# Performance work log

Measured on AMD Instinct MI355X. Metric: run time of the kernel, lower is better.

## Reference

```python
import jax, jax.numpy as jnp
import numpy as np

INF = 1e9
EPS = 1e-10
LN_EPS = 1e-5
H, CH = 8, 16  # no_heads, c_hidden


def setup_inputs() -> dict:
    key = jax.random.key(0)
    ks = jax.random.split(key, 8)
    B, S, R, C = 1, 2048, 512, 64  # batch, n_seq, n_res, c_in
    sc = 0.02
    m = jax.random.normal(ks[0], (B, S, R, C), jnp.float32)
    mask = jnp.ones((B, S, R), jnp.float32)
    ln_w = jnp.ones((C,), jnp.float32)
    ln_b = jnp.zeros((C,), jnp.float32)
    Wq = jax.random.normal(ks[1], (C, H * CH), jnp.float32) * sc
    Wk = jax.random.normal(ks[2], (C, CH), jnp.float32) * sc
    Wv = jax.random.normal(ks[3], (C, CH), jnp.float32) * sc
    Wg = jax.random.normal(ks[4], (C, H * CH), jnp.float32) * sc
    bg = jnp.ones((H * CH,), jnp.float32)  # gating init: bias = 1
    Wo = jax.random.normal(ks[5], (H * CH, C), jnp.float32) * sc
    bo = jnp.zeros((C,), jnp.float32)
    return {"m": m, "mask": mask, "ln_w": ln_w, "ln_b": ln_b, "Wq": Wq,
            "Wk": Wk, "Wv": Wv, "Wg": Wg, "bg": bg, "Wo": Wo, "bo": bo}


def reference(m, mask, ln_w, ln_b, Wq, Wk, Wv, Wg, bg, Wo, bo):
    # m: [B, S, R, C], mask: [B, S, R]
    m = jnp.swapaxes(m, -2, -3)        # [B, R, S, C] -- attend over seq per column
    mask = jnp.swapaxes(mask, -1, -2)  # [B, R, S]
    # LayerNorm over c_in
    mu = jnp.mean(m, axis=-1, keepdims=True)
    var = jnp.var(m, axis=-1, keepdims=True)
    mn = (m - mu) / jnp.sqrt(var + LN_EPS) * ln_w + ln_b  # [B, R, S, C]
    # masked mean-pooled query over seq dim
    q = jnp.sum(mn * mask[..., None], axis=-2) / (jnp.sum(mask, axis=-1)[..., None] + EPS)  # [B, R, C]
    q = (q @ Wq) * (CH ** -0.5)
    q = q.reshape(*q.shape[:-1], H, CH)  # [B, R, H, CH]
    k = mn @ Wk  # [B, R, S, CH]  (single shared K/V head)
    v = mn @ Wv  # [B, R, S, CH]
    a = jnp.einsum('brhc,brsc->brhs', q, k)
    a = a + (INF * (mask - 1.0))[..., None, :]  # additive mask bias
    a = jax.nn.softmax(a, axis=-1)               # [B, R, H, S]
    o = jnp.einsum('brhs,brsc->brhc', a, v)      # [B, R, H, CH]
    g = jax.nn.sigmoid(mn @ Wg + bg)             # [B, R, S, H*CH]
    g = g.reshape(*g.shape[:-1], H, CH)          # [B, R, S, H, CH]
    o = o[..., None, :, :] * g                   # broadcast pooled attn over seq
    o = o.reshape(*o.shape[:-2], -1)             # [B, R, S, H*CH]
    out = o @ Wo + bo                            # [B, R, S, C]
    return jnp.swapaxes(out, -2, -3)             # [B, S, R, C]
```

## Files before the change

### kernel.cpp

```cpp
#include <hip/hip_runtime.h>
#include <stdint.h>

#define S_ 2048
#define R_ 512
#define C_ 64
#define HC_ 128

typedef unsigned short u16;
typedef __attribute__((ext_vector_type(8))) short bf8_t;
typedef __attribute__((ext_vector_type(4))) float f4_t;

__device__ __forceinline__ u16 f2b(float f) {
    union { float f; unsigned int i; } x; x.f = f;
    unsigned int r = x.i + 0x7fffu + ((x.i >> 16) & 1u);
    return (u16)(r >> 16);
}
__device__ __forceinline__ float b2f(u16 u) {
    union { unsigned int i; float f; } x; x.i = ((unsigned int)u) << 16; return x.f;
}
__device__ __forceinline__ unsigned int pack2(float a, float b) {
    return (unsigned int)f2b(a) | ((unsigned int)f2b(b) << 16);
}
__device__ __forceinline__ void u4_to_f8(uint4 p, float* f) {
    union { unsigned int i; float f; } x;
    x.i = p.x << 16;         f[0] = x.f;
    x.i = p.x & 0xffff0000u; f[1] = x.f;
    x.i = p.y << 16;         f[2] = x.f;
    x.i = p.y & 0xffff0000u; f[3] = x.f;
    x.i = p.z << 16;         f[4] = x.f;
    x.i = p.z & 0xffff0000u; f[5] = x.f;
    x.i = p.w << 16;         f[6] = x.f;
    x.i = p.w & 0xffff0000u; f[7] = x.f;
}

__global__ __launch_bounds__(256) void k1a(
    const float* __restrict__ m, const float* __restrict__ mask,
    const float* __restrict__ lnw_g, const float* __restrict__ lnb_g,
    const float* __restrict__ Wk, const float* __restrict__ Wv,
    u16* __restrict__ kbuf, u16* __restrict__ vbuf,
    float* __restrict__ qsum, float* __restrict__ msum)
{
    __shared__ __attribute__((aligned(16))) u16 mns[32 * 72];
    __shared__ __attribute__((aligned(16))) u16 kvT[32 * 72];
    __shared__ __attribute__((aligned(16))) u16 kva[32 * 40];
    __shared__ float qred[4][64];
    __shared__ float msred[4];

    const int tid = threadIdx.x;
    const int bi  = blockIdx.x;
    const int r   = bi >> 6;
    const int s0  = (bi & 63) << 5;

    for (int idx = tid; idx < 2048; idx += 256) {
        int j = idx & 31, c = idx >> 5;
        float w = (j < 16) ? Wk[c * 16 + j] : Wv[c * 16 + (j - 16)];
        kvT[j * 72 + c] = f2b(w);
    }

    const int g = tid >> 4, l = tid & 15;
    const float4 lw4 = *(const float4*)&lnw_g[4 * l];
    const float4 lb4 = *(const float4*)&lnb_g[4 * l];

    float4 qacc = {0.f, 0.f, 0.f, 0.f};
    float msacc = 0.f;
    #pragma unroll
    for (int tt = 0; tt < 2; ++tt) {
        int t = g + tt * 16;
        int s = s0 + t;
        size_t base = ((size_t)s * R_ + r) * C_;
        float4 x = *(const float4*)&m[base + 4 * l];
        float sum = x.x + x.y + x.z + x.w;
        float ssq = x.x * x.x + x.y * x.y + x.z * x.z + x.w * x.w;
        #pragma unroll
        for (int off = 1; off <= 8; off <<= 1) {
            sum += __shfl_xor(sum, off);
            ssq += __shfl_xor(ssq, off);
        }
        float mu  = sum * (1.f / 64.f);
        float var = ssq * (1.f / 64.f) - mu * mu;
        float rs  = rsqrtf(var + 1e-5f);
        float4 mn;
        mn.x = (x.x - mu) * rs * lw4.x + lb4.x;
        mn.y = (x.y - mu) * rs * lw4.y + lb4.y;
        mn.z = (x.z - mu) * rs * lw4.z + lb4.z;
        mn.w = (x.w - mu) * rs * lw4.w + lb4.w;
        float mk = mask[(size_t)s * R_ + r];
        qacc.x += mn.x * mk; qacc.y += mn.y * mk;
        qacc.z += mn.z * mk; qacc.w += mn.w * mk;
        if (l == 0) msacc += mk;
        uint2 p; p.x = pack2(mn.x, mn.y); p.y = pack2(mn.z, mn.w);
        *(uint2*)&mns[t * 72 + 4 * l] = p;
    }
    qacc.x += __shfl_xor(qacc.x, 16); qacc.y += __shfl_xor(qacc.y, 16);
    qacc.z += __shfl_xor(qacc.z, 16); qacc.w += __shfl_xor(qacc.w, 16);
    qacc.x += __shfl_xor(qacc.x, 32); qacc.y += __shfl_xor(qacc.y, 32);
    qacc.z += __shfl_xor(qacc.z, 32); qacc.w += __shfl_xor(qacc.w, 32);
    msacc += __shfl_xor(msacc, 16);  msacc += __shfl_xor(msacc, 32);
    const int wv = tid >> 6, lane = tid & 63;
    if (lane < 16) *(float4*)&qred[wv][4 * lane] = qacc;
    if (lane == 0) msred[wv] = msacc;
    __syncthreads();

    {
        const int mt = wv & 1, nt = wv >> 1;
        const int r16 = lane & 15, quad = lane >> 4;
        f4_t acc = {0.f, 0.f, 0.f, 0.f};
        #pragma unroll
        for (int kt = 0; kt < 2; ++kt) {
            bf8_t a = *(const bf8_t*)&mns[(mt * 16 + r16) * 72 + kt * 32 + quad * 8];
            bf8_t b = *(const bf8_t*)&kvT[(nt * 16 + r16) * 72 + kt * 32 + quad * 8];
            acc = __builtin_amdgcn_mfma_f32_16x16x32_bf16(a, b, acc, 0, 0, 0);
        }
        #pragma unroll
        for (int i = 0; i < 4; ++i) {
            int row = mt * 16 + quad * 4 + i;
            kva[row * 40 + nt * 16 + r16] = f2b(acc[i]);
        }
    }
    __syncthreads();

    for (int uidx = tid; uidx < 512; uidx += 256) {
        int t = uidx >> 4, u = uidx & 15;
        unsigned int val = *(const unsigned int*)&kva[t * 40 + u * 2];
        int s = s0 + t;
        size_t tb = ((size_t)r * S_ + s) * 16;
        if (u < 8) *(unsigned int*)&kbuf[tb + u * 2] = val;
        else       *(unsigned int*)&vbuf[tb + (u - 8) * 2] = val;
    }
    if (tid < 64) {
        float tot = qred[0][tid] + qred[1][tid] + qred[2][tid] + qred[3][tid];
        atomicAdd(&qsum[r * 64 + tid], tot);
    }
    if (tid == 0) atomicAdd(&msum[r], msred[0] + msred[1] + msred[2] + msred[3]);
}

__global__ __launch_bounds__(256) void k1b(
    const float* __restrict__ qsum, const float* __restrict__ msum,
    const float* __restrict__ Wq, const float* __restrict__ mask,
    const u16* __restrict__ kbuf, const u16* __restrict__ vbuf,
    float* __restrict__ opool)
{
    __shared__ float qbar[64];
    __shared__ float qh[128];
    const int tid = threadIdx.x;
    const int r   = blockIdx.x;

    if (tid < 64) qbar[tid] = qsum[r * 64 + tid] / (msum[r] + 1e-10f);
    __syncthreads();
    if (tid < 128) {
        float a = 0.f;
        #pragma unroll 8
        for (int c = 0; c < 64; ++c) a += qbar[c] * Wq[c * 128 + tid];
        qh[tid] = a * 0.25f;
    }
    __syncthreads();

    const int wv = tid >> 6, lane = tid & 63;
    const int h0 = wv, h1 = wv + 4;
    float qa[16], qb[16];
    #pragma unroll
    for (int ch = 0; ch < 16; ++ch) { qa[ch] = qh[h0 * 16 + ch]; qb[ch] = qh[h1 * 16 + ch]; }

    float m0 = -1e30f, m1 = -1e30f;
    for (int i = 0; i < 32; ++i) {
        int s = i * 64 + lane;
        size_t tb = ((size_t)r * S_ + s) * 16;
        float kf[16];
        u4_to_f8(*(const uint4*)&kbuf[tb], kf);
        u4_to_f8(*(const uint4*)&kbuf[tb + 8], kf + 8);
        float bias = (mask[(size_t)s * R_ + r] - 1.f) * 1e9f;
        float a0 = bias, a1 = bias;
        #pragma unroll
        for (int ch = 0; ch < 16; ++ch) { a0 += qa[ch] * kf[ch]; a1 += qb[ch] * kf[ch]; }
        m0 = fmaxf(m0, a0); m1 = fmaxf(m1, a1);
    }
    #pragma unroll
    for (int off = 1; off < 64; off <<= 1) {
        m0 = fmaxf(m0, __shfl_xor(m0, off));
        m1 = fmaxf(m1, __shfl_xor(m1, off));
    }
    float l0 = 0.f, l1 = 0.f;
    float o0[16], o1[16];
    #pragma unroll
    for (int ch = 0; ch < 16; ++ch) { o0[ch] = 0.f; o1[ch] = 0.f; }
    for (int i = 0; i < 32; ++i) {
        int s = i * 64 + lane;
        size_t tb = ((size_t)r * S_ + s) * 16;
        float kf[16], vf[16];
        u4_to_f8(*(const uint4*)&kbuf[tb], kf);
        u4_to_f8(*(const uint4*)&kbuf[tb + 8], kf + 8);
        u4_to_f8(*(const uint4*)&vbuf[tb], vf);
        u4_to_f8(*(const uint4*)&vbuf[tb + 8], vf + 8);
        float bias = (mask[(size_t)s * R_ + r] - 1.f) * 1e9f;
        float a0 = bias, a1 = bias;
        #pragma unroll
        for (int ch = 0; ch < 16; ++ch) { a0 += qa[ch] * kf[ch]; a1 += qb[ch] * kf[ch]; }
        float w0 = expf(a0 - m0), w1 = expf(a1 - m1);
        l0 += w0; l1 += w1;
        #pragma unroll
        for (int ch = 0; ch < 16; ++ch) { o0[ch] += w0 * vf[ch]; o1[ch] += w1 * vf[ch]; }
    }
    #pragma unroll
    for (int off = 1; off < 64; off <<= 1) {
        l0 += __shfl_xor(l0, off); l1 += __shfl_xor(l1, off);
        #pragma unroll
        for (int ch = 0; ch < 16; ++ch) {
            o0[ch] += __shfl_xor(o0[ch], off);
            o1[ch] += __shfl_xor(o1[ch], off);
        }
    }
    if (lane == 0) {
        float inv0 = 1.f / l0, inv1 = 1.f / l1;
        #pragma unroll
        for (int ch = 0; ch < 16; ++ch) {
            opool[r * 128 + h0 * 16 + ch] = o0[ch] * inv0;
            opool[r * 128 + h1 * 16 + ch] = o1[ch] * inv1;
        }
    }
}

__global__ __launch_bounds__(256) void k2(
    const float* __restrict__ m,
    const float* __restrict__ lnw_g, const float* __restrict__ lnb_g,
    const float* __restrict__ Wg, const float* __restrict__ bg,
    const float* __restrict__ Wo, const float* __restrict__ bo,
    const float* __restrict__ opool, float* __restrict__ out)
{
    __shared__ __attribute__((aligned(16))) u16 WgT[128 * 72];
    __shared__ __attribute__((aligned(16))) u16 WoT[64 * 136];
    __shared__ __attribute__((aligned(16))) u16 mns[32 * 72];
    __shared__ __attribute__((aligned(16))) u16 olds[32 * 136];
    __shared__ __attribute__((aligned(16))) float outs[32 * 68];
    __shared__ float opl[128], bgl[128];
    __shared__ float bol[64];

    const int tid = threadIdx.x;
    const int bi  = blockIdx.x;
    const int r   = bi >> 6;
    const int s0  = (bi & 63) << 5;

    for (int idx = tid; idx < 8192; idx += 256) {
        int c = idx >> 7, hc = idx & 127;
        WgT[hc * 72 + c] = f2b(Wg[idx]);
    }
    for (int idx = tid; idx < 8192; idx += 256) {
        int hc = idx >> 6, c = idx & 63;
        WoT[c * 136 + hc] = f2b(Wo[idx]);
    }
    if (tid < 128) { opl[tid] = opool[r * 128 + tid]; bgl[tid] = bg[tid]; }
    if (tid < 64)  { bol[tid] = bo[tid]; }

    const int g = tid >> 4, l = tid & 15;
    const float4 lw4 = *(const float4*)&lnw_g[4 * l];
    const float4 lb4 = *(const float4*)&lnb_g[4 * l];
    #pragma unroll
    for (int tt = 0; tt < 2; ++tt) {
        int t = g + tt * 16;
        int s = s0 + t;
        size_t base = ((size_t)s * R_ + r) * C_;
        float4 x = *(const float4*)&m[base + 4 * l];
        float sum = x.x + x.y + x.z + x.w;
        float ssq = x.x * x.x + x.y * x.y + x.z * x.z + x.w * x.w;
        #pragma unroll
        for (int off = 1; off <= 8; off <<= 1) {
            sum += __shfl_xor(sum, off);
            ssq += __shfl_xor(ssq, off);
        }
        float mu  = sum * (1.f / 64.f);
        float var = ssq * (1.f / 64.f) - mu * mu;
        float rs  = rsqrtf(var + 1e-5f);
        uint2 p;
        p.x = pack2((x.x - mu) * rs * lw4.x + lb4.x, (x.y - mu) * rs * lw4.y + lb4.y);
        p.y = pack2((x.z - mu) * rs * lw4.z + lb4.z, (x.w - mu) * rs * lw4.w + lb4.w);
        *(uint2*)&mns[t * 72 + 4 * l] = p;
    }
    __syncthreads();

    const int wv = tid >> 6, lane = tid & 63;
    const int r16 = lane & 15, quad = lane >> 4;

    #pragma unroll
    for (int i = 0; i < 4; ++i) {
        int id = wv * 4 + i;
        int mt = id >> 3, nt = id & 7;
        f4_t acc = {0.f, 0.f, 0.f, 0.f};
        #pragma unroll
        for (int kt = 0; kt < 2; ++kt) {
            bf8_t a = *(const bf8_t*)&mns[(mt * 16 + r16) * 72 + kt * 32 + quad * 8];
            bf8_t b = *(const bf8_t*)&WgT[(nt * 16 + r16) * 72 + kt * 32 + quad * 8];
            acc = __builtin_amdgcn_mfma_f32_16x16x32_bf16(a, b, acc, 0, 0, 0);
        }
        int hc = nt * 16 + r16;
        float og = opl[hc], bgv = bgl[hc];
        #pragma unroll
        for (int ii = 0; ii < 4; ++ii) {
            int row = mt * 16 + quad * 4 + ii;
            float z  = acc[ii] + bgv;
            float gv = 1.f / (1.f + expf(-z));
            olds[row * 136 + hc] = f2b(og * gv);
        }
    }
    __syncthreads();

    #pragma unroll
    for (int i = 0; i < 2; ++i) {
        int id = wv * 2 + i;
        int mt = id >> 2, nt = id & 3;
        f4_t acc = {0.f, 0.f, 0.f, 0.f};
        #pragma unroll
        for (int kt = 0; kt < 4; ++kt) {
            bf8_t a = *(const bf8_t*)&olds[(mt * 16 + r16) * 136 + kt * 32 + quad * 8];
            bf8_t b = *(const bf8_t*)&WoT[(nt * 16 + r16) * 136 + kt * 32 + quad * 8];
            acc = __builtin_amdgcn_mfma_f32_16x16x32_bf16(a, b, acc, 0, 0, 0);
        }
        int c = nt * 16 + r16;
        float bov = bol[c];
        #pragma unroll
        for (int ii = 0; ii < 4; ++ii) {
            int row = mt * 16 + quad * 4 + ii;
            outs[row * 68 + c] = acc[ii] + bov;
        }
    }
    __syncthreads();

    #pragma unroll
    for (int tt = 0; tt < 2; ++tt) {
        int t = g + tt * 16;
        int s = s0 + t;
        size_t base = ((size_t)s * R_ + r) * C_;
        *(float4*)&out[base + 4 * l] = *(const float4*)&outs[t * 68 + 4 * l];
    }
}

extern "C" void kernel_launch(void* const* d_in, const int* in_sizes, int n_in,
                              void* d_out, int out_size, void* d_ws, size_t ws_size,
                              hipStream_t stream)
{
    const float* m    = (const float*)d_in[0];
    const float* mask = (const float*)d_in[1];
    const float* lnw  = (const float*)d_in[2];
    const float* lnb  = (const float*)d_in[3];
    const float* Wq   = (const float*)d_in[4];
    const float* Wk   = (const float*)d_in[5];
    const float* Wv   = (const float*)d_in[6];
    const float* Wg   = (const float*)d_in[7];
    const float* bg   = (const float*)d_in[8];
    const float* Wo   = (const float*)d_in[9];
    const float* bo   = (const float*)d_in[10];
    float* out = (float*)d_out;

    char* ws = (char*)d_ws;
    u16*   kbuf  = (u16*)ws;
    u16*   vbuf  = (u16*)(ws + (size_t)33554432);
    float* qsum  = (float*)(ws + (size_t)67108864);
    float* msum  = (float*)(ws + (size_t)67108864 + 131072);
    float* opool = (float*)(ws + (size_t)67108864 + 131072 + 2048);

    hipMemsetAsync(ws + (size_t)67108864, 0, 131072 + 2048, stream);
    k1a<<<32768, 256, 0, stream>>>(m, mask, lnw, lnb, Wk, Wv, kbuf, vbuf, qsum, msum);
    k1b<<<512, 256, 0, stream>>>(qsum, msum, Wq, mask, kbuf, vbuf, opool);
    k2<<<32768, 256, 0, stream>>>(m, lnw, lnb, Wg, bg, Wo, bo, opool, out);
}
```

Measured before the change: 1.029 ms.

## Pretranspose weights once and cache normalized activations for the gating kernel

Adds a small prologue kernel that converts and transposes Wk/Wv/Wg/Wo to bf16 once, instead of every block rebuilding them in shared memory. The attention kernels now load weight fragments straight into registers. When the workspace is large enough, k1a also writes the bf16 LayerNorm output to global memory, so the gating/output kernel reads 128 bytes per row instead of re-reading the fp32 input and redoing LayerNorm. This trades a 128MB extra write and read for less shared-memory setup and less LayerNorm work, and the path depends on the workspace size.

```diff
diff --git a/kernel.cpp b/kernel.cpp
--- a/kernel.cpp
+++ b/kernel.cpp
@@ -4,7 +4,6 @@
 #define S_ 2048
 #define R_ 512
 #define C_ 64
-#define HC_ 128
 
 typedef unsigned short u16;
 typedef __attribute__((ext_vector_type(8))) short bf8_t;
@@ -14,9 +13,6 @@
     union { float f; unsigned int i; } x; x.f = f;
     unsigned int r = x.i + 0x7fffu + ((x.i >> 16) & 1u);
     return (u16)(r >> 16);
-}
-__device__ __forceinline__ float b2f(u16 u) {
-    union { unsigned int i; float f; } x; x.i = ((unsigned int)u) << 16; return x.f;
 }
 __device__ __forceinline__ unsigned int pack2(float a, float b) {
     return (unsigned int)f2b(a) | ((unsigned int)f2b(b) << 16);
@@ -33,15 +29,36 @@
     x.i = p.w & 0xffff0000u; f[7] = x.f;
 }
 
+__global__ __launch_bounds__(256) void k0(
+    const float* __restrict__ Wk, const float* __restrict__ Wv,
+    const float* __restrict__ Wg, const float* __restrict__ Wo,
+    u16* __restrict__ kvT, u16* __restrict__ WgT, u16* __restrict__ WoT)
+{
+    int i = blockIdx.x * 256 + threadIdx.x;
+    if (i < 2048) {
+        int j = i >> 6, c = i & 63;
+        float w = (j < 16) ? Wk[c * 16 + j] : Wv[c * 16 + (j - 16)];
+        kvT[i] = f2b(w);
+    }
+    {
+        int hc = i >> 6, c = i & 63;
+        WgT[i] = f2b(Wg[c * 128 + hc]);
+    }
+    {
+        int c = i >> 7, hc = i & 127;
+        WoT[i] = f2b(Wo[hc * 64 + c]);
+    }
+}
+
 __global__ __launch_bounds__(256) void k1a(
     const float* __restrict__ m, const float* __restrict__ mask,
     const float* __restrict__ lnw_g, const float* __restrict__ lnb_g,
-    const float* __restrict__ Wk, const float* __restrict__ Wv,
+    const u16* __restrict__ kvT_g,
     u16* __restrict__ kbuf, u16* __restrict__ vbuf,
-    float* __restrict__ qsum, float* __restrict__ msum)
+    float* __restrict__ qsum, float* __restrict__ msum,
+    u16* __restrict__ mns_g)
 {
     __shared__ __attribute__((aligned(16))) u16 mns[32 * 72];
-    __shared__ __attribute__((aligned(16))) u16 kvT[32 * 72];
     __shared__ __attribute__((aligned(16))) u16 kva[32 * 40];
     __shared__ float qred[4][64];
     __shared__ float msred[4];
@@ -50,12 +67,12 @@
     const int bi  = blockIdx.x;
     const int r   = bi >> 6;
     const int s0  = (bi & 63) << 5;
-
-    for (int idx = tid; idx < 2048; idx += 256) {
-        int j = idx & 31, c = idx >> 5;
-        float w = (j < 16) ? Wk[c * 16 + j] : Wv[c * 16 + (j - 16)];
-        kvT[j * 72 + c] = f2b(w);
-    }
+    const int wv = tid >> 6, lane = tid & 63;
+    const int r16 = lane & 15, quad = lane >> 4;
+    const int mt = wv & 1, nt = wv >> 1;
+
+    bf8_t b0 = *(const bf8_t*)&kvT_g[(nt * 16 + r16) * 64 + quad * 8];
+    bf8_t b1 = *(const bf8_t*)&kvT_g[(nt * 16 + r16) * 64 + 32 + quad * 8];
 
     const int g = tid >> 4, l = tid & 15;
     const float4 lw4 = *(const float4*)&lnw_g[4 * l];
@@ -90,27 +107,24 @@
         if (l == 0) msacc += mk;
         uint2 p; p.x = pack2(mn.x, mn.y); p.y = pack2(mn.z, mn.w);
         *(uint2*)&mns[t * 72 + 4 * l] = p;
+        if (mns_g)
+            *(uint2*)&mns_g[((size_t)r * S_ + s) * C_ + 4 * l] = p;
     }
     qacc.x += __shfl_xor(qacc.x, 16); qacc.y += __shfl_xor(qacc.y, 16);
     qacc.z += __shfl_xor(qacc.z, 16); qacc.w += __shfl_xor(qacc.w, 16);
     qacc.x += __shfl_xor(qacc.x, 32); qacc.y += __shfl_xor(qacc.y, 32);
     qacc.z += __shfl_xor(qacc.z, 32); qacc.w += __shfl_xor(qacc.w, 32);
     msacc += __shfl_xor(msacc, 16);  msacc += __shfl_xor(msacc, 32);
-    const int wv = tid >> 6, lane = tid & 63;
     if (lane < 16) *(float4*)&qred[wv][4 * lane] = qacc;
     if (lane == 0) msred[wv] = msacc;
     __syncthreads();
 
     {
-        const int mt = wv & 1, nt = wv >> 1;
-        const int r16 = lane & 15, quad = lane >> 4;
         f4_t acc = {0.f, 0.f, 0.f, 0.f};
-        #pragma unroll
-        for (int kt = 0; kt < 2; ++kt) {
-            bf8_t a = *(const bf8_t*)&mns[(mt * 16 + r16) * 72 + kt * 32 + quad * 8];
-            bf8_t b = *(const bf8_t*)&kvT[(nt * 16 + r16) * 72 + kt * 32 + quad * 8];
-            acc = __builtin_amdgcn_mfma_f32_16x16x32_bf16(a, b, acc, 0, 0, 0);
-        }
+        bf8_t a0 = *(const bf8_t*)&mns[(mt * 16 + r16) * 72 + quad * 8];
+        bf8_t a1 = *(const bf8_t*)&mns[(mt * 16 + r16) * 72 + 32 + quad * 8];
+        acc = __builtin_amdgcn_mfma_f32_16x16x32_bf16(a0, b0, acc, 0, 0, 0);
+        acc = __builtin_amdgcn_mfma_f32_16x16x32_bf16(a1, b1, acc, 0, 0, 0);
         #pragma unroll
         for (int i = 0; i < 4; ++i) {
             int row = mt * 16 + quad * 4 + i;
@@ -219,15 +233,100 @@
     }
 }
 
-__global__ __launch_bounds__(256) void k2(
+__global__ __launch_bounds__(256) void k2m(
+    const u16* __restrict__ mns_g,
+    const u16* __restrict__ WgT_g, const u16* __restrict__ WoT_g,
+    const float* __restrict__ bg, const float* __restrict__ bo,
+    const float* __restrict__ opool, float* __restrict__ out)
+{
+    __shared__ __attribute__((aligned(16))) u16 olds[32 * 136];
+    __shared__ __attribute__((aligned(16))) float outs[32 * 68];
+    __shared__ float opl[128], bgl[128];
+    __shared__ float bol[64];
+
+    const int tid = threadIdx.x;
+    const int bi  = blockIdx.x;
+    const int r   = bi >> 6;
+    const int s0  = (bi & 63) << 5;
+    const int wv = tid >> 6, lane = tid & 63;
+    const int r16 = lane & 15, quad = lane >> 4;
+
+    const int mt  = wv >> 1;
+    const int nb2 = (wv & 1) * 4;
+    const int nb3 = (wv & 1) * 2;
+
+    bf8_t wg[4][2], wo[2][4];
+    #pragma unroll
+    for (int i = 0; i < 4; ++i)
+        #pragma unroll
+        for (int kt = 0; kt < 2; ++kt)
+            wg[i][kt] = *(const bf8_t*)&WgT_g[((nb2 + i) * 16 + r16) * 64 + kt * 32 + quad * 8];
+    #pragma unroll
+    for (int i = 0; i < 2; ++i)
+        #pragma unroll
+        for (int kt = 0; kt < 4; ++kt)
+            wo[i][kt] = *(const bf8_t*)&WoT_g[((nb3 + i) * 16 + r16) * 128 + kt * 32 + quad * 8];
+
+    size_t abase = ((size_t)r * S_ + s0 + mt * 16 + r16) * C_;
+    bf8_t a0 = *(const bf8_t*)&mns_g[abase + quad * 8];
+    bf8_t a1 = *(const bf8_t*)&mns_g[abase + 32 + quad * 8];
+
+    if (tid < 128) { opl[tid] = opool[r * 128 + tid]; bgl[tid] = bg[tid]; }
+    if (tid < 64)  { bol[tid] = bo[tid]; }
+    __syncthreads();
+
+    #pragma unroll
+    for (int i = 0; i < 4; ++i) {
+        f4_t acc = {0.f, 0.f, 0.f, 0.f};
+        acc = __builtin_amdgcn_mfma_f32_16x16x32_bf16(a0, wg[i][0], acc, 0, 0, 0);
+        acc = __builtin_amdgcn_mfma_f32_16x16x32_bf16(a1, wg[i][1], acc, 0, 0, 0);
+        int hc = (nb2 + i) * 16 + r16;
+        float og = opl[hc], bgv = bgl[hc];
+        #pragma unroll
+        for (int ii = 0; ii < 4; ++ii) {
+            int row = mt * 16 + quad * 4 + ii;
+            float z  = acc[ii] + bgv;
+            float gv = 1.f / (1.f + expf(-z));
+            olds[row * 136 + hc] = f2b(og * gv);
+        }
+    }
+    __syncthreads();
+
+    #pragma unroll
+    for (int i = 0; i < 2; ++i) {
+        f4_t acc = {0.f, 0.f, 0.f, 0.f};
+        #pragma unroll
+        for (int kt = 0; kt < 4; ++kt) {
+            bf8_t a = *(const bf8_t*)&olds[(mt * 16 + r16) * 136 + kt * 32 + quad * 8];
+            acc = __builtin_amdgcn_mfma_f32_16x16x32_bf16(a, wo[i][kt], acc, 0, 0, 0);
+        }
+        int c = (nb3 + i) * 16 + r16;
+        float bov = bol[c];
+        #pragma unroll
+        for (int ii = 0; ii < 4; ++ii) {
+            int row = mt * 16 + quad * 4 + ii;
+            outs[row * 68 + c] = acc[ii] + bov;
+        }
+    }
+    __syncthreads();
+
+    const int g = tid >> 4, l = tid & 15;
+    #pragma unroll
+    for (int tt = 0; tt < 2; ++tt) {
+        int t = g + tt * 16;
+        int s = s0 + t;
+        size_t base = ((size_t)s * R_ + r) * C_;
+        *(float4*)&out[base + 4 * l] = *(const float4*)&outs[t * 68 + 4 * l];
+    }
+}
+
+__global__ __launch_bounds__(256) void k2f(
     const float* __restrict__ m,
     const float* __restrict__ lnw_g, const float* __restrict__ lnb_g,
-    const float* __restrict__ Wg, const float* __restrict__ bg,
-    const float* __restrict__ Wo, const float* __restrict__ bo,
+    const u16* __restrict__ WgT_g, const u16* __restrict__ WoT_g,
+    const float* __restrict__ bg, const float* __restrict__ bo,
     const float* __restrict__ opool, float* __restrict__ out)
 {
-    __shared__ __attribute__((aligned(16))) u16 WgT[128 * 72];
-    __shared__ __attribute__((aligned(16))) u16 WoT[64 * 136];
     __shared__ __attribute__((aligned(16))) u16 mns[32 * 72];
     __shared__ __attribute__((aligned(16))) u16 olds[32 * 136];
     __shared__ __attribute__((aligned(16))) float outs[32 * 68];
@@ -238,15 +337,24 @@
     const int bi  = blockIdx.x;
     const int r   = bi >> 6;
     const int s0  = (bi & 63) << 5;
-
-    for (int idx = tid; idx < 8192; idx += 256) {
-        int c = idx >> 7, hc = idx & 127;
-        WgT[hc * 72 + c] = f2b(Wg[idx]);
-    }
-    for (int idx = tid; idx < 8192; idx += 256) {
-        int hc = idx >> 6, c = idx & 63;
-        WoT[c * 136 + hc] = f2b(Wo[idx]);
-    }
+    const int wv = tid >> 6, lane = tid & 63;
+    const int r16 = lane & 15, quad = lane >> 4;
+    const int mt  = wv >> 1;
+    const int nb2 = (wv & 1) * 4;
+    const int nb3 = (wv & 1) * 2;
+
+    bf8_t wg[4][2], wo[2][4];
+    #pragma unroll
+    for (int i = 0; i < 4; ++i)
+        #pragma unroll
+        for (int kt = 0; kt < 2; ++kt)
+            wg[i][kt] = *(const bf8_t*)&WgT_g[((nb2 + i) * 16 + r16) * 64 + kt * 32 + quad * 8];
+    #pragma unroll
+    for (int i = 0; i < 2; ++i)
+        #pragma unroll
+        for (int kt = 0; kt < 4; ++kt)
+            wo[i][kt] = *(const bf8_t*)&WoT_g[((nb3 + i) * 16 + r16) * 128 + kt * 32 + quad * 8];
+
     if (tid < 128) { opl[tid] = opool[r * 128 + tid]; bgl[tid] = bg[tid]; }
     if (tid < 64)  { bol[tid] = bo[tid]; }
 
@@ -276,21 +384,15 @@
     }
     __syncthreads();
 
-    const int wv = tid >> 6, lane = tid & 63;
-    const int r16 = lane & 15, quad = lane >> 4;
-
     #pragma unroll
     for (int i = 0; i < 4; ++i) {
-        int id = wv * 4 + i;
-        int mt = id >> 3, nt = id & 7;
         f4_t acc = {0.f, 0.f, 0.f, 0.f};
         #pragma unroll
         for (int kt = 0; kt < 2; ++kt) {
             bf8_t a = *(const bf8_t*)&mns[(mt * 16 + r16) * 72 + kt * 32 + quad * 8];
-            bf8_t b = *(const bf8_t*)&WgT[(nt * 16 + r16) * 72 + kt * 32 + quad * 8];
-            acc = __builtin_amdgcn_mfma_f32_16x16x32_bf16(a, b, acc, 0, 0, 0);
-        }
-        int hc = nt * 16 + r16;
+            acc = __builtin_amdgcn_mfma_f32_16x16x32_bf16(a, wg[i][kt], acc, 0, 0, 0);
+        }
+        int hc = (nb2 + i) * 16 + r16;
         float og = opl[hc], bgv = bgl[hc];
         #pragma unroll
         for (int ii = 0; ii < 4; ++ii) {
@@ -304,16 +406,13 @@
 
     #pragma unroll
     for (int i = 0; i < 2; ++i) {
-        int id = wv * 2 + i;
-        int mt = id >> 2, nt = id & 3;
         f4_t acc = {0.f, 0.f, 0.f, 0.f};
         #pragma unroll
         for (int kt = 0; kt < 4; ++kt) {
             bf8_t a = *(const bf8_t*)&olds[(mt * 16 + r16) * 136 + kt * 32 + quad * 8];
-            bf8_t b = *(const bf8_t*)&WoT[(nt * 16 + r16) * 136 + kt * 32 + quad * 8];
-            acc = __builtin_amdgcn_mfma_f32_16x16x32_bf16(a, b, acc, 0, 0, 0);
-        }
-        int c = nt * 16 + r16;
+            acc = __builtin_amdgcn_mfma_f32_16x16x32_bf16(a, wo[i][kt], acc, 0, 0, 0);
+        }
+        int c = (nb3 + i) * 16 + r16;
         float bov = bol[c];
         #pragma unroll
         for (int ii = 0; ii < 4; ++ii) {
@@ -351,13 +450,24 @@
 
     char* ws = (char*)d_ws;
     u16*   kbuf  = (u16*)ws;
-    u16*   vbuf  = (u16*)(ws + (size_t)33554432);
-    float* qsum  = (float*)(ws + (size_t)67108864);
-    float* msum  = (float*)(ws + (size_t)67108864 + 131072);
-    float* opool = (float*)(ws + (size_t)67108864 + 131072 + 2048);
-
-    hipMemsetAsync(ws + (size_t)67108864, 0, 131072 + 2048, stream);
-    k1a<<<32768, 256, 0, stream>>>(m, mask, lnw, lnb, Wk, Wv, kbuf, vbuf, qsum, msum);
+    u16*   vbuf  = (u16*)(ws + 33554432ull);
+    float* qsum  = (float*)(ws + 67108864ull);
+    float* msum  = (float*)(ws + 67239936ull);
+    float* opool = (float*)(ws + 67241984ull);
+    u16*   kvT   = (u16*)(ws + 67504128ull);
+    u16*   WgT   = (u16*)(ws + 67508224ull);
+    u16*   WoT   = (u16*)(ws + 67524608ull);
+    u16*   mns_g = (u16*)(ws + 67540992ull);
+    const size_t WS_NEED_MNS = 67540992ull + 134217728ull;
+    const bool use_mns = ws_size >= WS_NEED_MNS;
+
+    hipMemsetAsync(ws + 67108864ull, 0, 131072 + 2048, stream);
+    k0<<<32, 256, 0, stream>>>(Wk, Wv, Wg, Wo, kvT, WgT, WoT);
+    k1a<<<32768, 256, 0, stream>>>(m, mask, lnw, lnb, kvT, kbuf, vbuf, qsum, msum,
+                                   use_mns ? mns_g : (u16*)nullptr);
     k1b<<<512, 256, 0, stream>>>(qsum, msum, Wq, mask, kbuf, vbuf, opool);
-    k2<<<32768, 256, 0, stream>>>(m, lnw, lnb, Wg, bg, Wo, bo, opool, out);
-}
+    if (use_mns)
+        k2m<<<32768, 256, 0, stream>>>(mns_g, WgT, WoT, bg, bo, opool, out);
+    else
+        k2f<<<32768, 256, 0, stream>>>(m, lnw, lnb, WgT, WoT, bg, bo, opool, out);
+}
```

After: 849.2 us. 17.4% less time.
